# Kernel tuning notes

Measured on AMD Instinct MI355X. Metric: run time of the kernel, lower is better.

## Reference

```python
import jax, jax.numpy as jnp
import numpy as np

N = 6144
FEAT = 512
HID = 256
KMAX = 50
KNN = 20
SPATIAL_DECAY = 50.0
THR = 0.1


def setup_inputs() -> dict:
    key = jax.random.key(0)
    ks = jax.random.split(key, 4)
    features = jax.random.normal(ks[0], (N, FEAT), dtype=jnp.float32)
    # spatial coordinates in a ~1000um slide, matches spatial_decay=50
    positions = jax.random.uniform(ks[1], (N, 2), dtype=jnp.float32) * 1000.0
    W1 = jax.random.normal(ks[2], (FEAT, HID), dtype=jnp.float32) * np.float32(1.0 / np.sqrt(FEAT))
    b1 = jnp.zeros((HID,), jnp.float32)
    W2 = jax.random.normal(ks[3], (HID, KMAX), dtype=jnp.float32) * np.float32(1.0 / np.sqrt(HID))
    b2 = jnp.zeros((KMAX,), jnp.float32)
    return {
        "features": features,
        "positions": positions,
        "lambda_weight": jnp.asarray(0.5, jnp.float32),
        "temperature": jnp.asarray(1.0, jnp.float32),
        "spatial_weight": jnp.asarray(1.0, jnp.float32),
        "W1": W1, "b1": b1, "W2": W2, "b2": b2,
    }


def reference(features, positions, lambda_weight, temperature, spatial_weight, W1, b1, W2, b2):
    n = features.shape[0]
    # --- LearnableAdjacency (Eq. 6) ---
    norm = jnp.maximum(jnp.linalg.norm(features, axis=1, keepdims=True), 1e-12)
    fn = features / norm
    sim = fn @ fn.T                                  # [N,N]
    p2 = jnp.sum(positions * positions, axis=1)
    d2 = jnp.maximum(p2[:, None] + p2[None, :] - 2.0 * (positions @ positions.T), 0.0)
    spatial_k = jnp.exp(-d2 / (2.0 * SPATIAL_DECAY ** 2))
    lam = jax.nn.sigmoid(lambda_weight)
    adj = jax.nn.sigmoid((lam * sim + (1.0 - lam) * spatial_k) * temperature)
    # row-wise top-k mask (scatter of ones)
    _, topk_idx = jax.lax.top_k(adj, KNN)
    mask = jnp.zeros_like(adj).at[jnp.arange(n)[:, None], topk_idx].set(1.0)
    adj = adj * mask

    # --- edge_index <=> binary adjacency (threshold 0.1) ---
    A_bin = (adj > THR).astype(adj.dtype)            # edge pattern used by GCN + loss

    # --- DifferentiablePooling: 2-layer GCN over the edge pattern ---
    # PyG GCNConv: add self-loops (diag already 1 -> becomes 2), deg from target (col) sums,
    # edge norm d_r^{-1/2} d_c^{-1/2}, aggregate at target: out = Mn^T (X W) + b
    M = A_bin + jnp.eye(n, dtype=adj.dtype)
    dinv = jax.lax.rsqrt(jnp.sum(M, axis=0))
    Mn = (dinv[:, None] * M) * dinv[None, :]
    h = jax.nn.relu(Mn.T @ (features @ W1) + b1)
    s = Mn.T @ (h @ W2) + b2
    K = max(5, min(KMAX, int(np.ceil(N / 50))))      # static: 50
    S = jax.nn.softmax(s[:, :K], axis=1)             # [N,K]

    # --- spatial loss (Eq. 9), vectorized segment form ---
    # sum over edges (i,j): (S_i . S_j) * ||p_i - p_j||^2  == sum(S * ((A_bin*d2) @ S))
    E = jnp.sum(A_bin)
    We = A_bin * d2
    L_spatial = spatial_weight * jnp.sum(S * (We @ S)) / E

    # --- coarsening (Eq. 8) ---
    X_t = S.T @ features                             # [K,FEAT]
    A_coarse = S.T @ (adj @ S)                       # [K,K]
    A_t = A_coarse * (A_coarse > THR).astype(A_coarse.dtype)
    return (S, X_t, A_t, L_spatial, lam)
```

## Files before the change

kernel.cpp:

```cpp
#include <hip/hip_runtime.h>
#include <hip/hip_bf16.h>
#include <math.h>

#define N_PTS   6144
#define FEAT    512
#define HID     256
#define KMAX    50
#define KNN     20
#define THR     0.1f
#define CW      1536
#define NCHUNK  4

typedef unsigned short u16;
typedef __attribute__((ext_vector_type(8))) short bf16x8;
typedef __attribute__((ext_vector_type(8))) u16   u16x8;
typedef __attribute__((ext_vector_type(4))) float f32x4;

__device__ __forceinline__ u16 f2bf(float x) {
    union { float f; unsigned u; } a; a.f = x;
    unsigned r = (a.u + 0x7fffu + ((a.u >> 16) & 1u)) >> 16;
    return (u16)r;
}
__device__ __forceinline__ float bf2f(u16 h) {
    union { unsigned u; float f; } a; a.u = ((unsigned)h) << 16;
    return a.f;
}

__device__ __forceinline__ void gload16(const void* g, void* l) {
    __builtin_amdgcn_global_load_lds(
        (const __attribute__((address_space(1))) void*)g,
        (__attribute__((address_space(3))) void*)l, 16, 0, 0);
}

__global__ void init_kernel(int* __restrict__ indeg, int* __restrict__ fillc,
                            float* __restrict__ Ac, float* __restrict__ Xt,
                            int* __restrict__ ec) {
    int t = blockIdx.x * blockDim.x + threadIdx.x;
    if (t < N_PTS) { indeg[t] = 0; fillc[t] = 0; }
    if (t < KMAX * KMAX) Ac[t] = 0.f;
    if (t < KMAX * FEAT) Xt[t] = 0.f;
    if (t == 0) { ec[0] = 0; }
}

__global__ __launch_bounds__(64) void normalize_kernel(const float* __restrict__ f,
                                                       u16* __restrict__ fnh,
                                                       u16* __restrict__ fnl,
                                                       u16* __restrict__ fh_,
                                                       u16* __restrict__ fl_) {
    int row = blockIdx.x, lane = threadIdx.x;
    const float4* fr = (const float4*)(f + (size_t)row * FEAT);
    float4 v0 = fr[lane * 2 + 0];
    float4 v1 = fr[lane * 2 + 1];
    float ss = v0.x * v0.x + v0.y * v0.y + v0.z * v0.z + v0.w * v0.w
             + v1.x * v1.x + v1.y * v1.y + v1.z * v1.z + v1.w * v1.w;
#pragma unroll
    for (int m = 1; m < 64; m <<= 1) ss += __shfl_xor(ss, m);
    float nrm = fmaxf(sqrtf(ss), 1e-12f);
    float r[8] = { v0.x, v0.y, v0.z, v0.w, v1.x, v1.y, v1.z, v1.w };
    u16x8 h, l, rh, rl;
#pragma unroll
    for (int q = 0; q < 8; q++) {
        float vn = r[q] / nrm;
        u16 hb = f2bf(vn);
        h[q] = hb; l[q] = f2bf(vn - bf2f(hb));
        u16 rb = f2bf(r[q]);
        rh[q] = rb; rl[q] = f2bf(r[q] - bf2f(rb));
    }
    size_t base = (size_t)row * FEAT + lane * 8;
    *(u16x8*)(fnh + base) = h;
    *(u16x8*)(fnl + base) = l;
    *(u16x8*)(fh_ + base) = rh;
    *(u16x8*)(fl_ + base) = rl;
}

__global__ void p2_kernel(const float* __restrict__ pos, float* __restrict__ p2) {
    int i = blockIdx.x * blockDim.x + threadIdx.x;
    if (i < N_PTS) {
        float x = pos[2 * i], y = pos[2 * i + 1];
        p2[i] = x * x + y * y;
    }
}

__global__ __launch_bounds__(256) void w1t_split_kernel(const float* __restrict__ W1,
                                                        u16* __restrict__ th,
                                                        u16* __restrict__ tl) {
    int n = blockIdx.x;
    for (int k = threadIdx.x; k < FEAT; k += 256) {
        float v = W1[(size_t)k * HID + n];
        u16 hb = f2bf(v);
        th[(size_t)n * FEAT + k] = hb;
        tl[(size_t)n * FEAT + k] = f2bf(v - bf2f(hb));
    }
}

__global__ __launch_bounds__(256) void w2t_split_kernel(const float* __restrict__ W2,
                                                        u16* __restrict__ th,
                                                        u16* __restrict__ tl) {
    int n = blockIdx.x, k = threadIdx.x;
    float v = (n < KMAX) ? W2[(size_t)k * KMAX + n] : 0.f;
    u16 hb = f2bf(v);
    th[(size_t)n * HID + k] = hb;
    tl[(size_t)n * HID + k] = f2bf(v - bf2f(hb));
}

__global__ __launch_bounds__(256) void gemm_adj_mfma_kernel(
    const u16* __restrict__ fnh, const u16* __restrict__ fnl,
    const float* __restrict__ pos, const float* __restrict__ p2,
    const float* __restrict__ lamw, const float* __restrict__ tempw,
    float* __restrict__ out, int c0) {
    __shared__ u16 Ah[128 * 32], Al[128 * 32], Bh[128 * 32], Bl[128 * 32];
    const int tid  = threadIdx.x;
    const int lane = tid & 63, wid = tid >> 6;
    const int wm = wid >> 1, wn = wid & 1;
    const int bm  = blockIdx.y * 128;
    const int bnl = blockIdx.x * 128;
    const int bng = c0 + bnl;

    const u16* src; u16* dst; int grow;
    if      (wid == 0) { src = fnh; dst = Ah; grow = bm;  }
    else if (wid == 1) { src = fnl; dst = Al; grow = bm;  }
    else if (wid == 2) { src = fnh; dst = Bh; grow = bng; }
    else               { src = fnl; dst = Bl; grow = bng; }
    const u16* gbase = src + (size_t)(grow + (lane >> 2)) * FEAT + (lane & 3) * 8;

    f32x4 acc[4][4];
#pragma unroll
    for (int m = 0; m < 4; m++)
#pragma unroll
        for (int n = 0; n < 4; n++) acc[m][n] = (f32x4){0.f, 0.f, 0.f, 0.f};

    const int fr = lane & 15;
    const int ks = lane >> 4;
    const int abase = (wm * 64 + fr) * 32 + ks * 8;
    const int bbase = (wn * 64 + fr) * 32 + ks * 8;

    for (int k0 = 0; k0 < FEAT; k0 += 32) {
#pragma unroll
        for (int i = 0; i < 8; i++)
            gload16(gbase + k0 + (size_t)i * 16 * FEAT, dst + i * 512);
        __syncthreads();
        bf16x8 ahf[4], alf[4], bhf[4], blf[4];
#pragma unroll
        for (int m = 0; m < 4; m++) {
            ahf[m] = *(const bf16x8*)&Ah[abase + m * 16 * 32];
            alf[m] = *(const bf16x8*)&Al[abase + m * 16 * 32];
        }
#pragma unroll
        for (int n = 0; n < 4; n++) {
            bhf[n] = *(const bf16x8*)&Bh[bbase + n * 16 * 32];
            blf[n] = *(const bf16x8*)&Bl[bbase + n * 16 * 32];
        }
#pragma unroll
        for (int m = 0; m < 4; m++)
#pragma unroll
            for (int n = 0; n < 4; n++) {
                acc[m][n] = __builtin_amdgcn_mfma_f32_16x16x32_bf16(ahf[m], bhf[n], acc[m][n], 0, 0, 0);
                acc[m][n] = __builtin_amdgcn_mfma_f32_16x16x32_bf16(ahf[m], blf[n], acc[m][n], 0, 0, 0);
                acc[m][n] = __builtin_amdgcn_mfma_f32_16x16x32_bf16(alf[m], bhf[n], acc[m][n], 0, 0, 0);
            }
        __syncthreads();
    }

    float lam  = 1.f / (1.f + __expf(-lamw[0]));
    float temp = tempw[0];
    float p2c[4], pxc[4], pyc[4];
#pragma unroll
    for (int n = 0; n < 4; n++) {
        int cg = bng + wn * 64 + n * 16 + fr;
        p2c[n] = p2[cg]; pxc[n] = pos[2 * cg]; pyc[n] = pos[2 * cg + 1];
    }
#pragma unroll
    for (int m = 0; m < 4; m++) {
#pragma unroll
        for (int reg = 0; reg < 4; reg++) {
            int rrow = bm + wm * 64 + m * 16 + ks * 4 + reg;
            float p2r = p2[rrow], pxr = pos[2 * rrow], pyr = pos[2 * rrow + 1];
#pragma unroll
            for (int n = 0; n < 4; n++) {
                float sim = acc[m][n][reg];
                float d2 = fmaxf(p2r + p2c[n] - 2.f * (pxr * pxc[n] + pyr * pyc[n]), 0.f);
                float sk = __expf(-d2 * (1.f / 5000.f));
                float arg = (lam * sim + (1.f - lam) * sk) * temp;
                out[(size_t)rrow * CW + bnl + wn * 64 + n * 16 + fr] = 1.f / (1.f + __expf(-arg));
            }
        }
    }
}

__global__ __launch_bounds__(256) void gemm_z_kernel(
    const u16* __restrict__ xh, const u16* __restrict__ xl,
    const u16* __restrict__ w1th, const u16* __restrict__ w1tl,
    float* __restrict__ Z) {
    __shared__ u16 Ah[128 * 32], Al[128 * 32], Bh[128 * 32], Bl[128 * 32];
    const int tid  = threadIdx.x;
    const int lane = tid & 63, wid = tid >> 6;
    const int wm = wid >> 1, wn = wid & 1;
    const int bm = blockIdx.y * 128;
    const int bn = blockIdx.x * 128;

    const u16* src; u16* dst; int grow;
    if      (wid == 0) { src = xh;   dst = Ah; grow = bm; }
    else if (wid == 1) { src = xl;   dst = Al; grow = bm; }
    else if (wid == 2) { src = w1th; dst = Bh; grow = bn; }
    else               { src = w1tl; dst = Bl; grow = bn; }
    const u16* gbase = src + (size_t)(grow + (lane >> 2)) * FEAT + (lane & 3) * 8;

    f32x4 acc[4][4];
#pragma unroll
    for (int m = 0; m < 4; m++)
#pragma unroll
        for (int n = 0; n < 4; n++) acc[m][n] = (f32x4){0.f, 0.f, 0.f, 0.f};

    const int fr = lane & 15;
    const int ks = lane >> 4;
    const int abase = (wm * 64 + fr) * 32 + ks * 8;
    const int bbase = (wn * 64 + fr) * 32 + ks * 8;

    for (int k0 = 0; k0 < FEAT; k0 += 32) {
#pragma unroll
        for (int i = 0; i < 8; i++)
            gload16(gbase + k0 + (size_t)i * 16 * FEAT, dst + i * 512);
        __syncthreads();
        bf16x8 ahf[4], alf[4], bhf[4], blf[4];
#pragma unroll
        for (int m = 0; m < 4; m++) {
            ahf[m] = *(const bf16x8*)&Ah[abase + m * 16 * 32];
            alf[m] = *(const bf16x8*)&Al[abase + m * 16 * 32];
        }
#pragma unroll
        for (int n = 0; n < 4; n++) {
            bhf[n] = *(const bf16x8*)&Bh[bbase + n * 16 * 32];
            blf[n] = *(const bf16x8*)&Bl[bbase + n * 16 * 32];
        }
#pragma unroll
        for (int m = 0; m < 4; m++)
#pragma unroll
            for (int n = 0; n < 4; n++) {
                acc[m][n] = __builtin_amdgcn_mfma_f32_16x16x32_bf16(ahf[m], bhf[n], acc[m][n], 0, 0, 0);
                acc[m][n] = __builtin_amdgcn_mfma_f32_16x16x32_bf16(ahf[m], blf[n], acc[m][n], 0, 0, 0);
                acc[m][n] = __builtin_amdgcn_mfma_f32_16x16x32_bf16(alf[m], bhf[n], acc[m][n], 0, 0, 0);
            }
        __syncthreads();
    }
#pragma unroll
    for (int m = 0; m < 4; m++)
#pragma unroll
        for (int reg = 0; reg < 4; reg++) {
            int rrow = bm + wm * 64 + m * 16 + ks * 4 + reg;
#pragma unroll
            for (int n = 0; n < 4; n++)
                Z[(size_t)rrow * HID + bn + wn * 64 + n * 16 + fr] = acc[m][n][reg];
        }
}

__global__ __launch_bounds__(256) void gemm_y_kernel(
    const u16* __restrict__ hh, const u16* __restrict__ hl,
    const u16* __restrict__ w2th, const u16* __restrict__ w2tl,
    float* __restrict__ Y) {
    __shared__ u16 Ah[128 * 32], Al[128 * 32], Bh[64 * 32], Bl[64 * 32];
    const int tid  = threadIdx.x;
    const int lane = tid & 63, wid = tid >> 6;
    const int wm = wid >> 1, wn = wid & 1;
    const int bm = blockIdx.x * 128;

    const u16* src; u16* dst; int grow; int nld;
    if      (wid == 0) { src = hh;   dst = Ah; grow = bm; nld = 8; }
    else if (wid == 1) { src = hl;   dst = Al; grow = bm; nld = 8; }
    else if (wid == 2) { src = w2th; dst = Bh; grow = 0;  nld = 4; }
    else               { src = w2tl; dst = Bl; grow = 0;  nld = 4; }
    const u16* gbase = src + (size_t)(grow + (lane >> 2)) * HID + (lane & 3) * 8;

    f32x4 acc[4][2];
#pragma unroll
    for (int m = 0; m < 4; m++)
#pragma unroll
        for (int n = 0; n < 2; n++) acc[m][n] = (f32x4){0.f, 0.f, 0.f, 0.f};

    const int fr = lane & 15;
    const int ks = lane >> 4;
    const int abase = (wm * 64 + fr) * 32 + ks * 8;
    const int bbase = (wn * 32 + fr) * 32 + ks * 8;

    for (int k0 = 0; k0 < HID; k0 += 32) {
        for (int i = 0; i < nld; i++)
            gload16(gbase + k0 + (size_t)i * 16 * HID, dst + i * 512);
        __syncthreads();
        bf16x8 ahf[4], alf[4], bhf[2], blf[2];
#pragma unroll
        for (int m = 0; m < 4; m++) {
            ahf[m] = *(const bf16x8*)&Ah[abase + m * 16 * 32];
            alf[m] = *(const bf16x8*)&Al[abase + m * 16 * 32];
        }
#pragma unroll
        for (int n = 0; n < 2; n++) {
            bhf[n] = *(const bf16x8*)&Bh[bbase + n * 16 * 32];
            blf[n] = *(const bf16x8*)&Bl[bbase + n * 16 * 32];
        }
#pragma unroll
        for (int m = 0; m < 4; m++)
#pragma unroll
            for (int n = 0; n < 2; n++) {
                acc[m][n] = __builtin_amdgcn_mfma_f32_16x16x32_bf16(ahf[m], bhf[n], acc[m][n], 0, 0, 0);
                acc[m][n] = __builtin_amdgcn_mfma_f32_16x16x32_bf16(ahf[m], blf[n], acc[m][n], 0, 0, 0);
                acc[m][n] = __builtin_amdgcn_mfma_f32_16x16x32_bf16(alf[m], bhf[n], acc[m][n], 0, 0, 0);
            }
        __syncthreads();
    }
#pragma unroll
    for (int m = 0; m < 4; m++)
#pragma unroll
        for (int reg = 0; reg < 4; reg++) {
            int rrow = bm + wm * 64 + m * 16 + ks * 4 + reg;
#pragma unroll
            for (int n = 0; n < 2; n++) {
                int col = wn * 32 + n * 16 + fr;
                if (col < KMAX) Y[(size_t)rrow * KMAX + col] = acc[m][n][reg];
            }
        }
}

__global__ __launch_bounds__(256) void topk_kernel(const float* __restrict__ chunk,
                                                   float* __restrict__ gval,
                                                   int* __restrict__ gidx, int c0) {
    const int lane = threadIdx.x & 63;
    const int row  = blockIdx.x * 4 + (threadIdx.x >> 6);
    float lv = -INFINITY; int li = -1;
    if (c0 > 0 && lane < KNN) {
        lv = gval[(size_t)row * KNN + lane];
        li = gidx[(size_t)row * KNN + lane];
    }
    float T = __shfl(lv, KNN - 1);
    const float4* rp = (const float4*)(chunk + (size_t)row * CW);
    float4 q[CW / 256];
#pragma unroll
    for (int b = 0; b < CW / 256; b++) q[b] = rp[lane + 64 * b];
#pragma unroll
    for (int b = 0; b < CW / 256; b++) {
        float vv[4] = { q[b].x, q[b].y, q[b].z, q[b].w };
#pragma unroll
        for (int e = 0; e < 4; e++) {
            unsigned long long bal = __ballot(vv[e] > T);
            while (bal) {
                int src = __ffsll((unsigned long long)bal) - 1;
                bal &= bal - 1;
                float cv = __shfl(vv[e], src);
                if (cv > T) {
                    int cc = c0 + 4 * (src + 64 * b) + e;
                    float up = __shfl_up(lv, 1);
                    int  upi = __shfl_up(li, 1);
                    if (lane == 0) up = INFINITY;
                    bool keep = lv > cv;
                    float nv = keep ? lv : (up > cv ? cv : up);
                    int  ni = keep ? li : (up > cv ? cc : upi);
                    lv = nv; li = ni;
                    T = __shfl(lv, KNN - 1);
                }
            }
        }
    }
    if (lane < KNN) {
        gval[(size_t)row * KNN + lane] = lv;
        gidx[(size_t)row * KNN + lane] = li;
    }
}

__global__ void degree_kernel(const float* __restrict__ gval, const int* __restrict__ gidx,
                              int* __restrict__ indeg, int* __restrict__ ec) {
    int e = blockIdx.x * blockDim.x + threadIdx.x;
    bool pass = gval[e] > THR;
    if (pass) atomicAdd(&indeg[gidx[e]], 1);
    unsigned long long b = __ballot(pass);
    if ((threadIdx.x & 63) == 0) atomicAdd(ec, (int)__popcll(b));
}

__global__ __launch_bounds__(1024) void scan_kernel(const int* __restrict__ indeg,
                                                    int* __restrict__ offs,
                                                    float* __restrict__ dinv) {
    __shared__ int part[1024];
    int tid = threadIdx.x;
    int d[6], loc[6], s = 0;
#pragma unroll
    for (int q = 0; q < 6; q++) { d[q] = indeg[tid * 6 + q]; loc[q] = s; s += d[q]; }
    part[tid] = s;
    __syncthreads();
    for (int off = 1; off < 1024; off <<= 1) {
        int v = (tid >= off) ? part[tid - off] : 0;
        __syncthreads();
        part[tid] += v;
        __syncthreads();
    }
    int pre = (tid > 0) ? part[tid - 1] : 0;
#pragma unroll
    for (int q = 0; q < 6; q++) {
        offs[tid * 6 + q] = pre + loc[q];
        dinv[tid * 6 + q] = 1.0f / sqrtf((float)(d[q] + 1));
    }
    if (tid == 1023) offs[N_PTS] = part[1023];
}

__global__ void fill_kernel(const float* __restrict__ gval, const int* __restrict__ gidx,
                            const int* __restrict__ offs, int* __restrict__ fillc,
                            int* __restrict__ csc) {
    int e = blockIdx.x * blockDim.x + threadIdx.x;
    if (gval[e] > THR) {
        int j = gidx[e];
        int pos = offs[j] + atomicAdd(&fillc[j], 1);
        csc[pos] = e / KNN;
    }
}

__global__ __launch_bounds__(256) void agg1_kernel(const float* __restrict__ Z,
                                                   const int* __restrict__ offs,
                                                   const int* __restrict__ csc,
                                                   const float* __restrict__ dinv,
                                                   const float* __restrict__ b1,
                                                   u16* __restrict__ hh,
                                                   u16* __restrict__ hl) {
    int j = blockIdx.x, f = threadIdx.x;
    float dj = dinv[j];
    float acc = dj * Z[(size_t)j * HID + f];
    int e = offs[j], e1 = offs[j + 1];
    for (; e + 4 <= e1; e += 4) {
        int i0 = csc[e], i1 = csc[e + 1], i2 = csc[e + 2], i3 = csc[e + 3];
        float w0 = dinv[i0], w1 = dinv[i1], w2 = dinv[i2], w3 = dinv[i3];
        float z0 = Z[(size_t)i0 * HID + f], z1 = Z[(size_t)i1 * HID + f];
        float z2 = Z[(size_t)i2 * HID + f], z3 = Z[(size_t)i3 * HID + f];
        acc = fmaf(w0, z0, acc); acc = fmaf(w1, z1, acc);
        acc = fmaf(w2, z2, acc); acc = fmaf(w3, z3, acc);
    }
    for (; e < e1; e++) {
        int i = csc[e];
        acc = fmaf(dinv[i], Z[(size_t)i * HID + f], acc);
    }
    float hv = fmaxf(acc * dj + b1[f], 0.f);
    u16 hb = f2bf(hv);
    hh[(size_t)j * HID + f] = hb;
    hl[(size_t)j * HID + f] = f2bf(hv - bf2f(hb));
}

__global__ __launch_bounds__(64) void agg2_softmax_kernel(const float* __restrict__ Y,
                                                          const int* __restrict__ offs,
                                                          const int* __restrict__ csc,
                                                          const float* __restrict__ dinv,
                                                          const float* __restrict__ b2,
                                                          float* __restrict__ S) {
    int j = blockIdx.x, c = threadIdx.x;
    bool act = c < KMAX;
    float dj = dinv[j];
    float acc = act ? dj * Y[(size_t)j * KMAX + c] : 0.f;
    int e = offs[j], e1 = offs[j + 1];
    for (; e + 4 <= e1; e += 4) {
        int i0 = csc[e], i1 = csc[e + 1], i2 = csc[e + 2], i3 = csc[e + 3];
        float w0 = dinv[i0], w1 = dinv[i1], w2 = dinv[i2], w3 = dinv[i3];
        float y0 = act ? Y[(size_t)i0 * KMAX + c] : 0.f;
        float y1 = act ? Y[(size_t)i1 * KMAX + c] : 0.f;
        float y2 = act ? Y[(size_t)i2 * KMAX + c] : 0.f;
        float y3 = act ? Y[(size_t)i3 * KMAX + c] : 0.f;
        acc = fmaf(w0, y0, acc); acc = fmaf(w1, y1, acc);
        acc = fmaf(w2, y2, acc); acc = fmaf(w3, y3, acc);
    }
    for (; e < e1; e++) {
        int i = csc[e];
        if (act) acc = fmaf(dinv[i], Y[(size_t)i * KMAX + c], acc);
    }
    float s = act ? (acc * dj + b2[c]) : -INFINITY;
    float m = s;
#pragma unroll
    for (int msk = 1; msk < 64; msk <<= 1) m = fmaxf(m, __shfl_xor(m, msk));
    float ex = act ? expf(s - m) : 0.f;
    float tot = ex;
#pragma unroll
    for (int msk = 1; msk < 64; msk <<= 1) tot += __shfl_xor(tot, msk);
    if (act) S[(size_t)j * KMAX + c] = ex / tot;
}

__global__ __launch_bounds__(256) void rowops_kernel(const float* __restrict__ S,
                                                     const int* __restrict__ gidx,
                                                     const float* __restrict__ gval,
                                                     const float* __restrict__ pos,
                                                     const float* __restrict__ p2,
                                                     float* __restrict__ AS,
                                                     float* __restrict__ lossrow) {
    const int lane = threadIdx.x & 63;
    const int i = blockIdx.x * 4 + (threadIdx.x >> 6);
    const int c = lane;
    const bool act = c < KMAX;
    int jl = 0; float vl = 0.f, d2l = 0.f;
    if (lane < KNN) {
        jl = gidx[(size_t)i * KNN + lane];
        vl = gval[(size_t)i * KNN + lane];
        float pxi = pos[2 * i], pyi = pos[2 * i + 1], p2i = p2[i];
        d2l = fmaxf(p2i + p2[jl] - 2.f * (pxi * pos[2 * jl] + pyi * pos[2 * jl + 1]), 0.f);
    }
    float asum = 0.f, wsum = 0.f;
#pragma unroll
    for (int e = 0; e < KNN; e++) {
        int j = __shfl(jl, e);
        float v = __shfl(vl, e);
        float d2 = __shfl(d2l, e);
        float sv = act ? S[(size_t)j * KMAX + c] : 0.f;
        asum = fmaf(v, sv, asum);
        if (v > THR) wsum = fmaf(d2, sv, wsum);
    }
    if (act) AS[(size_t)i * KMAX + c] = asum;
    float li = act ? S[(size_t)i * KMAX + c] * wsum : 0.f;
#pragma unroll
    for (int m = 1; m < 64; m <<= 1) li += __shfl_xor(li, m);
    if (lane == 0) lossrow[i] = li;
}

__global__ __launch_bounds__(1024) void loss_reduce_kernel(const float* __restrict__ lossrow,
                                                           float* __restrict__ lossb) {
    int tid = threadIdx.x;
    float s = 0.f;
#pragma unroll
    for (int q = 0; q < 6; q++) s += lossrow[tid + 1024 * q];
#pragma unroll
    for (int m = 1; m < 64; m <<= 1) s += __shfl_xor(s, m);
    __shared__ float ws[16];
    if ((tid & 63) == 0) ws[tid >> 6] = s;
    __syncthreads();
    if (tid == 0) {
        float t = 0.f;
#pragma unroll
        for (int q = 0; q < 16; q++) t += ws[q];
        lossb[0] = t;
    }
}

__global__ __launch_bounds__(256) void coarseA_kernel(const float* __restrict__ S,
                                                      const float* __restrict__ AS,
                                                      float* __restrict__ Ac) {
    __shared__ float Ss[16][50];
    __shared__ float Bs[16][50];
    int tid = threadIdx.x;
    int n0 = blockIdx.x * 128;
    float acc[10];
    int ca[10], cb[10];
#pragma unroll
    for (int q = 0; q < 10; q++) {
        acc[q] = 0.f;
        int cell = tid + 256 * q;
        ca[q] = cell / 50; cb[q] = cell % 50;
    }
    for (int sub = 0; sub < 8; sub++) {
        int base = n0 + sub * 16;
        for (int idx = tid; idx < 16 * 50; idx += 256) {
            int r = idx / 50, c = idx % 50;
            Ss[r][c] = S[(size_t)(base + r) * KMAX + c];
            Bs[r][c] = AS[(size_t)(base + r) * KMAX + c];
        }
        __syncthreads();
        for (int r = 0; r < 16; r++) {
#pragma unroll
            for (int q = 0; q < 10; q++) {
                if (tid + 256 * q < 2500)
                    acc[q] = fmaf(Ss[r][ca[q]], Bs[r][cb[q]], acc[q]);
            }
        }
        __syncthreads();
    }
#pragma unroll
    for (int q = 0; q < 10; q++) {
        int cell = tid + 256 * q;
        if (cell < 2500) atomicAdd(&Ac[cell], acc[q]);
    }
}

__global__ __launch_bounds__(128) void coarseX_kernel(const float* __restrict__ S,
                                                      const float* __restrict__ X,
                                                      float* __restrict__ Xt) {
    __shared__ float Ss[16][50];
    int tid = threadIdx.x;
    int f = (blockIdx.x & 3) * 128 + tid;
    int n0 = (blockIdx.x >> 2) * 128;
    float acc[50];
#pragma unroll
    for (int a = 0; a < 50; a++) acc[a] = 0.f;
    for (int sub = 0; sub < 8; sub++) {
        int base = n0 + sub * 16;
        for (int idx = tid; idx < 16 * 50; idx += 128) {
            int r = idx / 50, c = idx % 50;
            Ss[r][c] = S[(size_t)(base + r) * KMAX + c];
        }
        __syncthreads();
        for (int r = 0; r < 16; r++) {
            float xv = X[(size_t)(base + r) * FEAT + f];
#pragma unroll
            for (int a = 0; a < 50; a++) acc[a] = fmaf(Ss[r][a], xv, acc[a]);
        }
        __syncthreads();
    }
#pragma unroll
    for (int a = 0; a < 50; a++) atomicAdd(&Xt[(size_t)a * FEAT + f], acc[a]);
}

__global__ void finalize_kernel(const float* __restrict__ Ac, const float* __restrict__ loss,
                                const int* __restrict__ ec, const float* __restrict__ sw,
                                const float* __restrict__ lamw, float* __restrict__ out_At,
                                float* __restrict__ out_scalars) {
    int t = blockIdx.x * blockDim.x + threadIdx.x;
    if (t < KMAX * KMAX) {
        float v = Ac[t];
        out_At[t] = (v > THR) ? v : 0.f;
    }
    if (t == 0) {
        out_scalars[0] = sw[0] * loss[0] / (float)ec[0];
        out_scalars[1] = 1.f / (1.f + expf(-lamw[0]));
    }
}

extern "C" void kernel_launch(void* const* d_in, const int* in_sizes, int n_in,
                              void* d_out, int out_size, void* d_ws, size_t ws_size,
                              hipStream_t stream) {
    const float* features = (const float*)d_in[0];
    const float* positions = (const float*)d_in[1];
    const float* lambda_w  = (const float*)d_in[2];
    const float* temp_w    = (const float*)d_in[3];
    const float* spatial_w = (const float*)d_in[4];
    const float* W1 = (const float*)d_in[5];
    const float* b1 = (const float*)d_in[6];
    const float* W2 = (const float*)d_in[7];
    const float* b2 = (const float*)d_in[8];

    float* out = (float*)d_out;
    float* out_S  = out;
    float* out_Xt = out + (size_t)N_PTS * KMAX;
    float* out_At = out_Xt + KMAX * FEAT;
    float* out_sc = out_At + KMAX * KMAX;

    char* ws = (char*)d_ws;
    size_t off = 0;
    auto alloc = [&](size_t bytes) { size_t o = off; off = (off + bytes + 255) & ~(size_t)255; return o; };
    u16*   fnh     = (u16*)  (ws + alloc((size_t)N_PTS * FEAT * 2));
    u16*   fnl     = (u16*)  (ws + alloc((size_t)N_PTS * FEAT * 2));
    u16*   fh      = (u16*)  (ws + alloc((size_t)N_PTS * FEAT * 2));
    u16*   fl      = (u16*)  (ws + alloc((size_t)N_PTS * FEAT * 2));
    float* p2      = (float*)(ws + alloc((size_t)N_PTS * 4));
    float* adjchnk = (float*)(ws + alloc((size_t)N_PTS * CW * 4));
    float* gval    = (float*)(ws + alloc((size_t)N_PTS * KNN * 4));
    int*   gidx    = (int*)  (ws + alloc((size_t)N_PTS * KNN * 4));
    int*   indeg   = (int*)  (ws + alloc((size_t)N_PTS * 4));
    int*   fillc   = (int*)  (ws + alloc((size_t)N_PTS * 4));
    int*   offs    = (int*)  (ws + alloc((size_t)(N_PTS + 1) * 4));
    float* dinv    = (float*)(ws + alloc((size_t)N_PTS * 4));
    int*   csc     = (int*)  (ws + alloc((size_t)N_PTS * KNN * 4));
    u16*   w1th    = (u16*)  (ws + alloc((size_t)HID * FEAT * 2));
    u16*   w1tl    = (u16*)  (ws + alloc((size_t)HID * FEAT * 2));
    u16*   w2th    = (u16*)  (ws + alloc((size_t)64 * HID * 2));
    u16*   w2tl    = (u16*)  (ws + alloc((size_t)64 * HID * 2));
    float* lossrow = (float*)(ws + alloc((size_t)N_PTS * 4));
    float* Ac      = (float*)(ws + alloc((size_t)KMAX * KMAX * 4));
    float* lossb   = (float*)(ws + alloc(4));
    int*   ecnt    = (int*)  (ws + alloc(4));

    char* ov = (char*)adjchnk;
    float* Z  = (float*)(ov);
    u16*   hh = (u16*)  (ov + 7 * 1024 * 1024);
    u16*   hl = (u16*)  (ov + 11 * 1024 * 1024);
    float* Y  = (float*)(ov + 15 * 1024 * 1024);
    float* AS = (float*)(ov + 17 * 1024 * 1024);

    init_kernel<<<(KMAX * FEAT + 255) / 256, 256, 0, stream>>>(indeg, fillc, Ac, out_Xt, ecnt);
    normalize_kernel<<<N_PTS, 64, 0, stream>>>(features, fnh, fnl, fh, fl);
    p2_kernel<<<(N_PTS + 255) / 256, 256, 0, stream>>>(positions, p2);
    w1t_split_kernel<<<HID, 256, 0, stream>>>(W1, w1th, w1tl);
    w2t_split_kernel<<<64, 256, 0, stream>>>(W2, w2th, w2tl);
    for (int c = 0; c < NCHUNK; c++) {
        gemm_adj_mfma_kernel<<<dim3(CW / 128, N_PTS / 128), 256, 0, stream>>>(
            fnh, fnl, positions, p2, lambda_w, temp_w, adjchnk, c * CW);
        topk_kernel<<<N_PTS / 4, 256, 0, stream>>>(adjchnk, gval, gidx, c * CW);
    }
    degree_kernel<<<(N_PTS * KNN) / 256, 256, 0, stream>>>(gval, gidx, indeg, ecnt);
    scan_kernel<<<1, 1024, 0, stream>>>(indeg, offs, dinv);
    fill_kernel<<<(N_PTS * KNN) / 256, 256, 0, stream>>>(gval, gidx, offs, fillc, csc);
    gemm_z_kernel<<<dim3(HID / 128, N_PTS / 128), 256, 0, stream>>>(fh, fl, w1th, w1tl, Z);
    agg1_kernel<<<N_PTS, HID, 0, stream>>>(Z, offs, csc, dinv, b1, hh, hl);
    gemm_y_kernel<<<N_PTS / 128, 256, 0, stream>>>(hh, hl, w2th, w2tl, Y);
    agg2_softmax_kernel<<<N_PTS, 64, 0, stream>>>(Y, offs, csc, dinv, b2, out_S);
    rowops_kernel<<<N_PTS / 4, 256, 0, stream>>>(out_S, gidx, gval, positions, p2, AS, lossrow);
    loss_reduce_kernel<<<1, 1024, 0, stream>>>(lossrow, lossb);
    coarseA_kernel<<<N_PTS / 128, 256, 0, stream>>>(out_S, AS, Ac);
    coarseX_kernel<<<(N_PTS / 128) * 4, 128, 0, stream>>>(out_S, features, out_Xt);
    finalize_kernel<<<(KMAX * KMAX + 255) / 256, 256, 0, stream>>>(Ac, lossb, ecnt, spatial_w, lambda_w, out_At, out_sc);
}
```

Before: 559.3 us.

## Swizzle LDS layout and workgroup order in GEMMs, pack agg2 rows per block

The three MFMA GEMM kernels now XOR-swizzle the k-chunk position when writing and reading shared memory, which is meant to cut LDS bank conflicts on fragment reads. The adjacency and Z GEMMs also remap the flat block index in groups of eight, likely to spread neighbouring tiles across XCDs or improve L2 locality. The agg2 softmax kernel packs four rows into each 256-thread block instead of one 64-thread block per row, reducing launch and scheduling overhead. The swizzle has to match the unseen MFMA read pattern exactly, and the block remap assumes the grid size divides by eight.

```diff
diff --git a/kernel.cpp b/kernel.cpp
--- a/kernel.cpp
+++ b/kernel.cpp
@@ -103,6 +103,7 @@
     tl[(size_t)n * HID + k] = f2bf(v - bf2f(hb));
 }
 
+
 __global__ __launch_bounds__(256) void gemm_adj_mfma_kernel(
     const u16* __restrict__ fnh, const u16* __restrict__ fnl,
     const float* __restrict__ pos, const float* __restrict__ p2,
@@ -112,8 +113,12 @@
     const int tid  = threadIdx.x;
     const int lane = tid & 63, wid = tid >> 6;
     const int wm = wid >> 1, wn = wid & 1;
-    const int bm  = blockIdx.y * 128;
-    const int bnl = blockIdx.x * 128;
+    const int flat = blockIdx.y * gridDim.x + blockIdx.x;
+    const int nwg  = gridDim.x * gridDim.y;
+    const int swzb = (flat & 7) * (nwg >> 3) + (flat >> 3);
+    const int bx = swzb % gridDim.x, by = swzb / gridDim.x;
+    const int bm  = by * 128;
+    const int bnl = bx * 128;
     const int bng = c0 + bnl;
 
     const u16* src; u16* dst; int grow;
@@ -121,7 +126,8 @@
     else if (wid == 1) { src = fnl; dst = Al; grow = bm;  }
     else if (wid == 2) { src = fnh; dst = Bh; grow = bng; }
     else               { src = fnl; dst = Bl; grow = bng; }
-    const u16* gbase = src + (size_t)(grow + (lane >> 2)) * FEAT + (lane & 3) * 8;
+    const u16* gbase = src + (size_t)(grow + (lane >> 2)) * FEAT
+                     + (((lane & 3) ^ ((lane >> 3) & 3)) * 8);
 
     f32x4 acc[4][4];
 #pragma unroll
@@ -131,8 +137,9 @@
 
     const int fr = lane & 15;
     const int ks = lane >> 4;
-    const int abase = (wm * 64 + fr) * 32 + ks * 8;
-    const int bbase = (wn * 64 + fr) * 32 + ks * 8;
+    const int ksw = (ks ^ ((fr >> 1) & 3)) * 8;
+    const int abase = (wm * 64 + fr) * 32 + ksw;
+    const int bbase = (wn * 64 + fr) * 32 + ksw;
 
     for (int k0 = 0; k0 < FEAT; k0 += 32) {
 #pragma unroll
@@ -195,15 +202,19 @@
     const int tid  = threadIdx.x;
     const int lane = tid & 63, wid = tid >> 6;
     const int wm = wid >> 1, wn = wid & 1;
-    const int bm = blockIdx.y * 128;
-    const int bn = blockIdx.x * 128;
+    const int flat = blockIdx.y * gridDim.x + blockIdx.x;
+    const int nwg  = gridDim.x * gridDim.y;
+    const int swzb = (flat & 7) * (nwg >> 3) + (flat >> 3);
+    const int bm = (swzb / gridDim.x) * 128;
+    const int bn = (swzb % gridDim.x) * 128;
 
     const u16* src; u16* dst; int grow;
     if      (wid == 0) { src = xh;   dst = Ah; grow = bm; }
     else if (wid == 1) { src = xl;   dst = Al; grow = bm; }
     else if (wid == 2) { src = w1th; dst = Bh; grow = bn; }
     else               { src = w1tl; dst = Bl; grow = bn; }
-    const u16* gbase = src + (size_t)(grow + (lane >> 2)) * FEAT + (lane & 3) * 8;
+    const u16* gbase = src + (size_t)(grow + (lane >> 2)) * FEAT
+                     + (((lane & 3) ^ ((lane >> 3) & 3)) * 8);
 
     f32x4 acc[4][4];
 #pragma unroll
@@ -213,8 +224,9 @@
 
     const int fr = lane & 15;
     const int ks = lane >> 4;
-    const int abase = (wm * 64 + fr) * 32 + ks * 8;
-    const int bbase = (wn * 64 + fr) * 32 + ks * 8;
+    const int ksw = (ks ^ ((fr >> 1) & 3)) * 8;
+    const int abase = (wm * 64 + fr) * 32 + ksw;
+    const int bbase = (wn * 64 + fr) * 32 + ksw;
 
     for (int k0 = 0; k0 < FEAT; k0 += 32) {
 #pragma unroll
@@ -268,7 +280,8 @@
     else if (wid == 1) { src = hl;   dst = Al; grow = bm; nld = 8; }
     else if (wid == 2) { src = w2th; dst = Bh; grow = 0;  nld = 4; }
     else               { src = w2tl; dst = Bl; grow = 0;  nld = 4; }
-    const u16* gbase = src + (size_t)(grow + (lane >> 2)) * HID + (lane & 3) * 8;
+    const u16* gbase = src + (size_t)(grow + (lane >> 2)) * HID
+                     + (((lane & 3) ^ ((lane >> 3) & 3)) * 8);
 
     f32x4 acc[4][2];
 #pragma unroll
@@ -278,8 +291,9 @@
 
     const int fr = lane & 15;
     const int ks = lane >> 4;
-    const int abase = (wm * 64 + fr) * 32 + ks * 8;
-    const int bbase = (wn * 32 + fr) * 32 + ks * 8;
+    const int ksw = (ks ^ ((fr >> 1) & 3)) * 8;
+    const int abase = (wm * 64 + fr) * 32 + ksw;
+    const int bbase = (wn * 32 + fr) * 32 + ksw;
 
     for (int k0 = 0; k0 < HID; k0 += 32) {
         for (int i = 0; i < nld; i++)
@@ -438,13 +452,14 @@
     hl[(size_t)j * HID + f] = f2bf(hv - bf2f(hb));
 }
 
-__global__ __launch_bounds__(64) void agg2_softmax_kernel(const float* __restrict__ Y,
-                                                          const int* __restrict__ offs,
-                                                          const int* __restrict__ csc,
-                                                          const float* __restrict__ dinv,
-                                                          const float* __restrict__ b2,
-                                                          float* __restrict__ S) {
-    int j = blockIdx.x, c = threadIdx.x;
+__global__ __launch_bounds__(256) void agg2_softmax_kernel(const float* __restrict__ Y,
+                                                           const int* __restrict__ offs,
+                                                           const int* __restrict__ csc,
+                                                           const float* __restrict__ dinv,
+                                                           const float* __restrict__ b2,
+                                                           float* __restrict__ S) {
+    int c = threadIdx.x & 63;
+    int j = blockIdx.x * 4 + (threadIdx.x >> 6);
     bool act = c < KMAX;
     float dj = dinv[j];
     float acc = act ? dj * Y[(size_t)j * KMAX + c] : 0.f;
@@ -677,7 +692,7 @@
     gemm_z_kernel<<<dim3(HID / 128, N_PTS / 128), 256, 0, stream>>>(fh, fl, w1th, w1tl, Z);
     agg1_kernel<<<N_PTS, HID, 0, stream>>>(Z, offs, csc, dinv, b1, hh, hl);
     gemm_y_kernel<<<N_PTS / 128, 256, 0, stream>>>(hh, hl, w2th, w2tl, Y);
-    agg2_softmax_kernel<<<N_PTS, 64, 0, stream>>>(Y, offs, csc, dinv, b2, out_S);
+    agg2_softmax_kernel<<<N_PTS / 4, 256, 0, stream>>>(Y, offs, csc, dinv, b2, out_S);
     rowops_kernel<<<N_PTS / 4, 256, 0, stream>>>(out_S, gidx, gval, positions, p2, AS, lossrow);
     loss_reduce_kernel<<<1, 1024, 0, stream>>>(lossrow, lossb);
     coarseA_kernel<<<N_PTS / 128, 256, 0, stream>>>(out_S, AS, Ac);
```

New measurement: 550.2 us. No clear change (-1.6%).
